# Kernel optimization log

Measured on AMD Instinct MI355X. Metric: run time of the kernel, lower is better.

The kernel has to match this reference:

```python
import jax, jax.numpy as jnp
import numpy as np

N_NODES = 10000
N_EDGES = 160000
D = 512
DROPOUT_P = 0.5
NEG_SLOPE = 0.25


def setup_inputs() -> dict:
    key = jax.random.key(0)
    ks = jax.random.split(key, 8)
    H = jax.random.normal(ks[0], (N_NODES, D), dtype=jnp.float32)
    rows = jax.random.randint(ks[1], (N_EDGES,), 0, N_NODES)
    cols = jax.random.randint(ks[2], (N_EDGES,), 0, N_NODES)
    vals = jax.random.uniform(ks[3], (N_EDGES,), dtype=jnp.float32)
    # xavier-normal-ish weights, zero bias (matches torch init)
    std = float(np.sqrt(2.0 / (D + D)))
    W1 = jax.random.normal(ks[4], (D, D), dtype=jnp.float32) * std
    b1 = jnp.zeros((D,), dtype=jnp.float32)
    W2 = jax.random.normal(ks[5], (D, D), dtype=jnp.float32) * std
    b2 = jnp.zeros((D,), dtype=jnp.float32)
    return {"H": H, "rows": rows, "cols": cols, "vals": vals,
            "W1": W1, "b1": b1, "W2": W2, "b2": b2}


def _spmm(rows, cols, vals, dense):
    # sparse [N,N] @ dense [N,D] via gather + segment-sum
    gathered = vals[:, None] * dense[cols]          # [E, D]
    return jax.ops.segment_sum(gathered, rows, num_segments=N_NODES)


def _leaky_relu(x):
    return jnp.where(x >= 0, x, NEG_SLOPE * x)


def reference(H, rows, cols, vals, W1, b1, W2, b2):
    # layer 1: dense GEMM -> SpMM -> bias -> leaky_relu -> dropout(training=True)
    h = _spmm(rows, cols, vals, H @ W1) + b1
    h = _leaky_relu(h)
    keep = jax.random.bernoulli(jax.random.key(42), 1.0 - DROPOUT_P, h.shape)
    h = jnp.where(keep, h / (1.0 - DROPOUT_P), 0.0)
    # layer 2
    h = _spmm(rows, cols, vals, h @ W2) + b2
    return _leaky_relu(h)
```

## Files before the change

### kernel.cpp

```cpp
#include <hip/hip_runtime.h>
#include <stdint.h>

#define N_NODES 10000
#define M_PAD   10112
#define N_EDGES 160000
#define DIM     512
#define N_ELEMS 5120000
#define NEG_SLOPE 0.25f

typedef short     short8 __attribute__((ext_vector_type(8)));
typedef __bf16    bf16x8 __attribute__((ext_vector_type(8)));
typedef float     f32x4  __attribute__((ext_vector_type(4)));

__device__ __forceinline__ unsigned short f2bf(float f) {
    uint32_t u = __builtin_bit_cast(uint32_t, f);
    uint32_t r = (u + 0x7fffu + ((u >> 16) & 1u)) >> 16;
    return (unsigned short)r;
}
__device__ __forceinline__ float b2f(unsigned short u) {
    return __builtin_bit_cast(float, (uint32_t)u << 16);
}

__device__ __forceinline__ uint32_t rotl32(uint32_t x, uint32_t d) {
    return (x << d) | (x >> (32u - d));
}
__device__ __forceinline__ void threefry_42(uint32_t x0, uint32_t x1,
                                            uint32_t& o0, uint32_t& o1) {
    const uint32_t ks0 = 0u, ks1 = 42u, ks2 = 0x1BD11BDAu ^ 42u;
    x0 += ks0; x1 += ks1;
#define TF_R4(a,b,c,d) \
    x0 += x1; x1 = rotl32(x1,a); x1 ^= x0; \
    x0 += x1; x1 = rotl32(x1,b); x1 ^= x0; \
    x0 += x1; x1 = rotl32(x1,c); x1 ^= x0; \
    x0 += x1; x1 = rotl32(x1,d); x1 ^= x0;
    TF_R4(13,15,26,6);  x0 += ks1; x1 += ks2 + 1u;
    TF_R4(17,29,16,24); x0 += ks2; x1 += ks0 + 2u;
    TF_R4(13,15,26,6);  x0 += ks0; x1 += ks1 + 3u;
    TF_R4(17,29,16,24); x0 += ks1; x1 += ks2 + 4u;
    TF_R4(13,15,26,6);  x0 += ks2; x1 += ks0 + 5u;
#undef TF_R4
    o0 = x0; o1 = x1;
}

__global__ void hist_kernel(const int* __restrict__ rows, int* __restrict__ cnt) {
    int e = blockIdx.x * blockDim.x + threadIdx.x;
    if (e < N_EDGES) atomicAdd(&cnt[rows[e]], 1);
}

__global__ __launch_bounds__(1024)
void scan_kernel(const int* __restrict__ cnt, int* __restrict__ rs, int* __restrict__ cur) {
    __shared__ int s[1024];
    int t = threadIdx.x;
    int base_i = t * 10;
    int local[10];
    int p = 0;
    if (t < 1000) {
        #pragma unroll
        for (int j = 0; j < 10; ++j) { local[j] = cnt[base_i + j]; p += local[j]; }
    }
    s[t] = p;
    __syncthreads();
    for (int off = 1; off < 1024; off <<= 1) {
        int v = (t >= off) ? s[t - off] : 0;
        __syncthreads();
        s[t] += v;
        __syncthreads();
    }
    if (t < 1000) {
        int run = s[t] - p;
        #pragma unroll
        for (int j = 0; j < 10; ++j) {
            rs[base_i + j]  = run;
            cur[base_i + j] = run;
            run += local[j];
        }
        if (t == 999) rs[N_NODES] = run;
    }
}

__global__ void scatter_kernel(const int* __restrict__ rows, const int* __restrict__ cols,
                               const float* __restrict__ vals, int* __restrict__ cur,
                               int* __restrict__ scol, float* __restrict__ sval) {
    int e = blockIdx.x * blockDim.x + threadIdx.x;
    if (e < N_EDGES) {
        int r = rows[e];
        int p = atomicAdd(&cur[r], 1);
        scol[p] = cols[e];
        sval[p] = vals[e];
    }
}

__global__ void convert_kernel(const float* __restrict__ src, unsigned short* __restrict__ dst) {
    int i = blockIdx.x * blockDim.x + threadIdx.x;
    if (i * 4 >= N_ELEMS) return;
    float4 v = ((const float4*)src)[i];
    ushort4 o;
    o.x = f2bf(v.x); o.y = f2bf(v.y); o.z = f2bf(v.z); o.w = f2bf(v.w);
    ((ushort4*)dst)[i] = o;
}

__global__ __launch_bounds__(256)
void transpose_kernel(const float* __restrict__ W, unsigned short* __restrict__ WT) {
    __shared__ float t[64][65];
    int k0 = blockIdx.x * 64, n0 = blockIdx.y * 64;
    int tx = threadIdx.x & 15, ty = threadIdx.x >> 4;
    #pragma unroll
    for (int i = 0; i < 4; ++i) {
        int k = i * 16 + ty;
        float4 v = *(const float4*)&W[(size_t)(k0 + k) * DIM + n0 + tx * 4];
        t[k][tx * 4 + 0] = v.x; t[k][tx * 4 + 1] = v.y;
        t[k][tx * 4 + 2] = v.z; t[k][tx * 4 + 3] = v.w;
    }
    __syncthreads();
    #pragma unroll
    for (int i = 0; i < 4; ++i) {
        int n = i * 16 + ty;
        ushort4 o;
        o.x = f2bf(t[tx * 4 + 0][n]); o.y = f2bf(t[tx * 4 + 1][n]);
        o.z = f2bf(t[tx * 4 + 2][n]); o.w = f2bf(t[tx * 4 + 3][n]);
        *(ushort4*)&WT[(size_t)(n0 + n) * DIM + k0 + tx * 4] = o;
    }
}

__global__ __launch_bounds__(256)
void mfma_gemm(const unsigned short* __restrict__ A, const unsigned short* __restrict__ BT,
               unsigned short* __restrict__ C, int M) {
    __shared__ short8 As[1024];
    __shared__ short8 Bs[1024];
    int tid  = threadIdx.x;
    int wid  = tid >> 6, lane = tid & 63;
    int bm   = blockIdx.x * 128;
    int bn   = blockIdx.y * 128;
    int wm   = (wid >> 1) * 64, wn = (wid & 1) * 64;

    f32x4 acc[4][4] = {};

    int srow = lane >> 3;
    int sslot = lane & 7;

    for (int k0 = 0; k0 < DIM; k0 += 64) {
        #pragma unroll
        for (int c = 0; c < 4; ++c) {
            int chunk = wid * 4 + c;
            int r  = chunk * 8 + srow;
            int ks = sslot ^ (r & 7);
            const unsigned short* ga = A  + (size_t)(bm + r) * DIM + k0 + ks * 8;
            const unsigned short* gb = BT + (size_t)(bn + r) * DIM + k0 + ks * 8;
            __builtin_amdgcn_global_load_lds(
                (const __attribute__((address_space(1))) void*)ga,
                (__attribute__((address_space(3))) void*)&As[chunk * 64], 16, 0, 0);
            __builtin_amdgcn_global_load_lds(
                (const __attribute__((address_space(1))) void*)gb,
                (__attribute__((address_space(3))) void*)&Bs[chunk * 64], 16, 0, 0);
        }
        __syncthreads();

        int lrow = lane & 15;
        int kgrp = lane >> 4;
        #pragma unroll
        for (int ks = 0; ks < 2; ++ks) {
            short8 af[4], bfr[4];
            #pragma unroll
            for (int i = 0; i < 4; ++i) {
                int r = wm + i * 16 + lrow;
                af[i]  = As[r * 8 + ((ks * 4 + kgrp) ^ (r & 7))];
                int n = wn + i * 16 + lrow;
                bfr[i] = Bs[n * 8 + ((ks * 4 + kgrp) ^ (n & 7))];
            }
            #pragma unroll
            for (int i = 0; i < 4; ++i)
                #pragma unroll
                for (int j = 0; j < 4; ++j)
                    acc[i][j] = __builtin_amdgcn_mfma_f32_16x16x32_bf16(
                        __builtin_bit_cast(bf16x8, af[i]),
                        __builtin_bit_cast(bf16x8, bfr[j]), acc[i][j], 0, 0, 0);
        }
        __syncthreads();
    }

    int crow = (lane >> 4) * 4;
    int ccol = lane & 15;
    #pragma unroll
    for (int i = 0; i < 4; ++i) {
        #pragma unroll
        for (int r = 0; r < 4; ++r) {
            int row = bm + wm + i * 16 + crow + r;
            if (row < M) {
                size_t base = (size_t)row * DIM + bn + wn + ccol;
                #pragma unroll
                for (int j = 0; j < 4; ++j)
                    C[base + j * 16] = f2bf(acc[i][j][r]);
            }
        }
    }
}

__global__ __launch_bounds__(128)
void spmm1_kernel(const unsigned short* __restrict__ X, const int* __restrict__ rs,
                  const int* __restrict__ scol, const float* __restrict__ sval,
                  const float* __restrict__ bias, unsigned short* __restrict__ hout) {
    int row = blockIdx.x;
    int t = threadIdx.x;
    int start = rs[row], end = rs[row + 1];
    const ushort4* X4 = (const ushort4*)X;
    float a0 = 0.f, a1 = 0.f, a2 = 0.f, a3 = 0.f;
    float c0 = 0.f, c1 = 0.f, c2 = 0.f, c3 = 0.f;
    int p = start;
    for (; p + 1 < end; p += 2) {
        int   i0 = scol[p], i1 = scol[p + 1];
        float v0 = sval[p], v1 = sval[p + 1];
        ushort4 x0 = X4[(size_t)i0 * 128 + t];
        ushort4 x1 = X4[(size_t)i1 * 128 + t];
        a0 = fmaf(v0, b2f(x0.x), a0); a1 = fmaf(v0, b2f(x0.y), a1);
        a2 = fmaf(v0, b2f(x0.z), a2); a3 = fmaf(v0, b2f(x0.w), a3);
        c0 = fmaf(v1, b2f(x1.x), c0); c1 = fmaf(v1, b2f(x1.y), c1);
        c2 = fmaf(v1, b2f(x1.z), c2); c3 = fmaf(v1, b2f(x1.w), c3);
    }
    if (p < end) {
        int i0 = scol[p]; float v0 = sval[p];
        ushort4 x0 = X4[(size_t)i0 * 128 + t];
        a0 = fmaf(v0, b2f(x0.x), a0); a1 = fmaf(v0, b2f(x0.y), a1);
        a2 = fmaf(v0, b2f(x0.z), a2); a3 = fmaf(v0, b2f(x0.w), a3);
    }
    float r[4];
    float4 b = *(const float4*)&bias[t * 4];
    r[0] = a0 + c0 + b.x; r[1] = a1 + c1 + b.y;
    r[2] = a2 + c2 + b.z; r[3] = a3 + c3 + b.w;
    uint32_t e0 = (uint32_t)row * DIM + t * 4;
    #pragma unroll
    for (int j = 0; j < 4; ++j) {
        float v = r[j];
        v = (v >= 0.f) ? v : NEG_SLOPE * v;
        uint32_t o0, o1;
        threefry_42(0u, e0 + j, o0, o1);
        uint32_t bits = o0 ^ o1;
        r[j] = ((int)bits >= 0) ? v * 2.0f : 0.0f;
    }
    ushort4 o;
    o.x = f2bf(r[0]); o.y = f2bf(r[1]); o.z = f2bf(r[2]); o.w = f2bf(r[3]);
    ((ushort4*)hout)[(size_t)row * 128 + t] = o;
}

__global__ __launch_bounds__(128)
void spmm2_kernel(const unsigned short* __restrict__ X, const int* __restrict__ rs,
                  const int* __restrict__ scol, const float* __restrict__ sval,
                  const float* __restrict__ bias, float* __restrict__ out) {
    int row = blockIdx.x;
    int t = threadIdx.x;
    int start = rs[row], end = rs[row + 1];
    const ushort4* X4 = (const ushort4*)X;
    float a0 = 0.f, a1 = 0.f, a2 = 0.f, a3 = 0.f;
    float c0 = 0.f, c1 = 0.f, c2 = 0.f, c3 = 0.f;
    int p = start;
    for (; p + 1 < end; p += 2) {
        int   i0 = scol[p], i1 = scol[p + 1];
        float v0 = sval[p], v1 = sval[p + 1];
        ushort4 x0 = X4[(size_t)i0 * 128 + t];
        ushort4 x1 = X4[(size_t)i1 * 128 + t];
        a0 = fmaf(v0, b2f(x0.x), a0); a1 = fmaf(v0, b2f(x0.y), a1);
        a2 = fmaf(v0, b2f(x0.z), a2); a3 = fmaf(v0, b2f(x0.w), a3);
        c0 = fmaf(v1, b2f(x1.x), c0); c1 = fmaf(v1, b2f(x1.y), c1);
        c2 = fmaf(v1, b2f(x1.z), c2); c3 = fmaf(v1, b2f(x1.w), c3);
    }
    if (p < end) {
        int i0 = scol[p]; float v0 = sval[p];
        ushort4 x0 = X4[(size_t)i0 * 128 + t];
        a0 = fmaf(v0, b2f(x0.x), a0); a1 = fmaf(v0, b2f(x0.y), a1);
        a2 = fmaf(v0, b2f(x0.z), a2); a3 = fmaf(v0, b2f(x0.w), a3);
    }
    float4 b = *(const float4*)&bias[t * 4];
    float4 r;
    r.x = a0 + c0 + b.x; r.y = a1 + c1 + b.y;
    r.z = a2 + c2 + b.z; r.w = a3 + c3 + b.w;
    r.x = (r.x >= 0.f) ? r.x : NEG_SLOPE * r.x;
    r.y = (r.y >= 0.f) ? r.y : NEG_SLOPE * r.y;
    r.z = (r.z >= 0.f) ? r.z : NEG_SLOPE * r.z;
    r.w = (r.w >= 0.f) ? r.w : NEG_SLOPE * r.w;
    ((float4*)out)[(size_t)row * 128 + t] = r;
}

extern "C" void kernel_launch(void* const* d_in, const int* in_sizes, int n_in,
                              void* d_out, int out_size, void* d_ws, size_t ws_size,
                              hipStream_t stream) {
    const float* H    = (const float*)d_in[0];
    const int*   rows = (const int*)  d_in[1];
    const int*   cols = (const int*)  d_in[2];
    const float* vals = (const float*)d_in[3];
    const float* W1   = (const float*)d_in[4];
    const float* b1   = (const float*)d_in[5];
    const float* W2   = (const float*)d_in[6];
    const float* b2   = (const float*)d_in[7];
    float* out = (float*)d_out;

    char* ws = (char*)d_ws;
    size_t off = 0;
    auto alloc = [&](size_t bytes) -> void* {
        off = (off + 255) & ~(size_t)255;
        void* p = ws + off;
        off += bytes;
        return p;
    };
    int*   cnt  = (int*)  alloc((size_t)N_NODES * 4);
    int*   rs   = (int*)  alloc((size_t)(N_NODES + 1) * 4);
    int*   cur  = (int*)  alloc((size_t)N_NODES * 4);
    int*   scol = (int*)  alloc((size_t)N_EDGES * 4);
    float* sval = (float*)alloc((size_t)N_EDGES * 4);
    unsigned short* WT1 = (unsigned short*)alloc((size_t)DIM * DIM * 2);
    unsigned short* WT2 = (unsigned short*)alloc((size_t)DIM * DIM * 2);
    unsigned short* Abf = (unsigned short*)alloc((size_t)M_PAD * DIM * 2);
    unsigned short* hbf = (unsigned short*)alloc((size_t)M_PAD * DIM * 2);
    unsigned short* Xbf = (unsigned short*)alloc((size_t)N_NODES * DIM * 2);

    convert_kernel<<<(N_ELEMS / 4 + 255) / 256, 256, 0, stream>>>(H, Abf);
    dim3 tgrid(DIM / 64, DIM / 64);
    transpose_kernel<<<tgrid, 256, 0, stream>>>(W1, WT1);
    transpose_kernel<<<tgrid, 256, 0, stream>>>(W2, WT2);
    hipMemsetAsync(cnt, 0, (size_t)N_NODES * 4, stream);
    hist_kernel<<<(N_EDGES + 255) / 256, 256, 0, stream>>>(rows, cnt);
    scan_kernel<<<1, 1024, 0, stream>>>(cnt, rs, cur);
    scatter_kernel<<<(N_EDGES + 255) / 256, 256, 0, stream>>>(rows, cols, vals, cur, scol, sval);

    dim3 ggrid(M_PAD / 128, DIM / 128);
    mfma_gemm<<<ggrid, 256, 0, stream>>>(Abf, WT1, Xbf, N_NODES);
    spmm1_kernel<<<N_NODES, 128, 0, stream>>>(Xbf, rs, scol, sval, b1, hbf);
    mfma_gemm<<<ggrid, 256, 0, stream>>>(hbf, WT2, Xbf, N_NODES);
    spmm2_kernel<<<N_NODES, 128, 0, stream>>>(Xbf, rs, scol, sval, b2, out);
}
```

Before: 126.9 us.

## Fuse prep kernels, precompute dropout mask, shrink GEMM tile, wave-per-row SpMM

```diff
diff --git a/kernel.cpp b/kernel.cpp
--- a/kernel.cpp
+++ b/kernel.cpp
@@ -8,9 +8,10 @@
 #define N_ELEMS 5120000
 #define NEG_SLOPE 0.25f
 
-typedef short     short8 __attribute__((ext_vector_type(8)));
-typedef __bf16    bf16x8 __attribute__((ext_vector_type(8)));
-typedef float     f32x4  __attribute__((ext_vector_type(4)));
+typedef short          short8   __attribute__((ext_vector_type(8)));
+typedef unsigned short ushort8v __attribute__((ext_vector_type(8)));
+typedef __bf16         bf16x8   __attribute__((ext_vector_type(8)));
+typedef float          f32x4    __attribute__((ext_vector_type(4)));
 
 __device__ __forceinline__ unsigned short f2bf(float f) {
     uint32_t u = __builtin_bit_cast(uint32_t, f);
@@ -42,6 +43,71 @@
     o0 = x0; o1 = x1;
 }
 
+#define CONV_BLKS 5000
+#define TR_BLKS   64
+#define MASK_BLKS 625
+#define ZERO_BLKS 10
+
+__device__ __forceinline__ void transpose_tile(const float* __restrict__ W,
+                                               unsigned short* __restrict__ WT,
+                                               int tile, float (*ts)[65]) {
+    int k0 = (tile & 7) * 64, n0 = (tile >> 3) * 64;
+    int tx = threadIdx.x & 15, ty = threadIdx.x >> 4;
+    #pragma unroll
+    for (int i = 0; i < 4; ++i) {
+        int k = i * 16 + ty;
+        float4 v = *(const float4*)&W[(size_t)(k0 + k) * DIM + n0 + tx * 4];
+        ts[k][tx * 4 + 0] = v.x; ts[k][tx * 4 + 1] = v.y;
+        ts[k][tx * 4 + 2] = v.z; ts[k][tx * 4 + 3] = v.w;
+    }
+    __syncthreads();
+    #pragma unroll
+    for (int i = 0; i < 4; ++i) {
+        int n = i * 16 + ty;
+        ushort4 o;
+        o.x = f2bf(ts[tx * 4 + 0][n]); o.y = f2bf(ts[tx * 4 + 1][n]);
+        o.z = f2bf(ts[tx * 4 + 2][n]); o.w = f2bf(ts[tx * 4 + 3][n]);
+        *(ushort4*)&WT[(size_t)(n0 + n) * DIM + k0 + tx * 4] = o;
+    }
+}
+
+__global__ __launch_bounds__(256)
+void prep_kernel(const float* __restrict__ H, const float* __restrict__ W1,
+                 const float* __restrict__ W2, unsigned short* __restrict__ Abf,
+                 unsigned short* __restrict__ WT1, unsigned short* __restrict__ WT2,
+                 uint32_t* __restrict__ mask, int* __restrict__ cnt) {
+    __shared__ float ts[64][65];
+    int b = blockIdx.x;
+    if (b < CONV_BLKS) {
+        int i = b * 256 + threadIdx.x;
+        float4 v = ((const float4*)H)[i];
+        ushort4 o;
+        o.x = f2bf(v.x); o.y = f2bf(v.y); o.z = f2bf(v.z); o.w = f2bf(v.w);
+        ((ushort4*)Abf)[i] = o;
+    } else if (b < CONV_BLKS + TR_BLKS) {
+        transpose_tile(W1, WT1, b - CONV_BLKS, ts);
+    } else if (b < CONV_BLKS + 2 * TR_BLKS) {
+        transpose_tile(W2, WT2, b - CONV_BLKS - TR_BLKS, ts);
+    } else if (b < CONV_BLKS + 2 * TR_BLKS + MASK_BLKS) {
+        int w = (b - CONV_BLKS - 2 * TR_BLKS) * 256 + threadIdx.x;
+        uint32_t base = (uint32_t)w * 32;
+        uint32_t m = 0;
+        #pragma unroll
+        for (int j = 0; j < 32; ++j) {
+            uint32_t o0, o1;
+            threefry_42(0u, base + j, o0, o1);
+            uint32_t bits = o0 ^ o1;
+            m |= (uint32_t)(((int)bits >= 0) ? 1u : 0u) << j;
+        }
+        mask[w] = m;
+    } else {
+        int i = (b - CONV_BLKS - 2 * TR_BLKS - MASK_BLKS) * 1024 + threadIdx.x * 4;
+        #pragma unroll
+        for (int j = 0; j < 4; ++j)
+            if (i + j < N_NODES) cnt[i + j] = 0;
+    }
+}
+
 __global__ void hist_kernel(const int* __restrict__ rows, int* __restrict__ cnt) {
     int e = blockIdx.x * blockDim.x + threadIdx.x;
     if (e < N_EDGES) atomicAdd(&cnt[rows[e]], 1);
@@ -90,68 +156,40 @@
     }
 }
 
-__global__ void convert_kernel(const float* __restrict__ src, unsigned short* __restrict__ dst) {
-    int i = blockIdx.x * blockDim.x + threadIdx.x;
-    if (i * 4 >= N_ELEMS) return;
-    float4 v = ((const float4*)src)[i];
-    ushort4 o;
-    o.x = f2bf(v.x); o.y = f2bf(v.y); o.z = f2bf(v.z); o.w = f2bf(v.w);
-    ((ushort4*)dst)[i] = o;
-}
-
-__global__ __launch_bounds__(256)
-void transpose_kernel(const float* __restrict__ W, unsigned short* __restrict__ WT) {
-    __shared__ float t[64][65];
-    int k0 = blockIdx.x * 64, n0 = blockIdx.y * 64;
-    int tx = threadIdx.x & 15, ty = threadIdx.x >> 4;
-    #pragma unroll
-    for (int i = 0; i < 4; ++i) {
-        int k = i * 16 + ty;
-        float4 v = *(const float4*)&W[(size_t)(k0 + k) * DIM + n0 + tx * 4];
-        t[k][tx * 4 + 0] = v.x; t[k][tx * 4 + 1] = v.y;
-        t[k][tx * 4 + 2] = v.z; t[k][tx * 4 + 3] = v.w;
-    }
-    __syncthreads();
-    #pragma unroll
-    for (int i = 0; i < 4; ++i) {
-        int n = i * 16 + ty;
-        ushort4 o;
-        o.x = f2bf(t[tx * 4 + 0][n]); o.y = f2bf(t[tx * 4 + 1][n]);
-        o.z = f2bf(t[tx * 4 + 2][n]); o.w = f2bf(t[tx * 4 + 3][n]);
-        *(ushort4*)&WT[(size_t)(n0 + n) * DIM + k0 + tx * 4] = o;
-    }
-}
-
 __global__ __launch_bounds__(256)
 void mfma_gemm(const unsigned short* __restrict__ A, const unsigned short* __restrict__ BT,
                unsigned short* __restrict__ C, int M) {
-    __shared__ short8 As[1024];
-    __shared__ short8 Bs[1024];
+    __shared__ short8 As[128 * 8];
+    __shared__ short8 Bs[64 * 8];
     int tid  = threadIdx.x;
     int wid  = tid >> 6, lane = tid & 63;
     int bm   = blockIdx.x * 128;
-    int bn   = blockIdx.y * 128;
-    int wm   = (wid >> 1) * 64, wn = (wid & 1) * 64;
-
-    f32x4 acc[4][4] = {};
-
-    int srow = lane >> 3;
-    int sslot = lane & 7;
+    int bn   = blockIdx.y * 64;
+    int wm   = (wid >> 1) * 64, wn = (wid & 1) * 32;
+
+    f32x4 acc[4][2] = {};
+    int srow = lane >> 3, sslot = lane & 7;
 
     for (int k0 = 0; k0 < DIM; k0 += 64) {
         #pragma unroll
         for (int c = 0; c < 4; ++c) {
-            int chunk = wid * 4 + c;
-            int r  = chunk * 8 + srow;
+            int r0 = c * 32 + wid * 8;
+            int r  = r0 + srow;
             int ks = sslot ^ (r & 7);
-            const unsigned short* ga = A  + (size_t)(bm + r) * DIM + k0 + ks * 8;
+            const unsigned short* ga = A + (size_t)(bm + r) * DIM + k0 + ks * 8;
+            __builtin_amdgcn_global_load_lds(
+                (const __attribute__((address_space(1))) void*)ga,
+                (__attribute__((address_space(3))) void*)&As[r0 * 8], 16, 0, 0);
+        }
+        #pragma unroll
+        for (int c = 0; c < 2; ++c) {
+            int r0 = c * 32 + wid * 8;
+            int r  = r0 + srow;
+            int ks = sslot ^ (r & 7);
             const unsigned short* gb = BT + (size_t)(bn + r) * DIM + k0 + ks * 8;
             __builtin_amdgcn_global_load_lds(
-                (const __attribute__((address_space(1))) void*)ga,
-                (__attribute__((address_space(3))) void*)&As[chunk * 64], 16, 0, 0);
-            __builtin_amdgcn_global_load_lds(
                 (const __attribute__((address_space(1))) void*)gb,
-                (__attribute__((address_space(3))) void*)&Bs[chunk * 64], 16, 0, 0);
+                (__attribute__((address_space(3))) void*)&Bs[r0 * 8], 16, 0, 0);
         }
         __syncthreads();
 
@@ -159,18 +197,21 @@
         int kgrp = lane >> 4;
         #pragma unroll
         for (int ks = 0; ks < 2; ++ks) {
-            short8 af[4], bfr[4];
+            short8 af[4], bfr[2];
             #pragma unroll
             for (int i = 0; i < 4; ++i) {
                 int r = wm + i * 16 + lrow;
-                af[i]  = As[r * 8 + ((ks * 4 + kgrp) ^ (r & 7))];
-                int n = wn + i * 16 + lrow;
-                bfr[i] = Bs[n * 8 + ((ks * 4 + kgrp) ^ (n & 7))];
+                af[i] = As[r * 8 + ((ks * 4 + kgrp) ^ (r & 7))];
+            }
+            #pragma unroll
+            for (int j = 0; j < 2; ++j) {
+                int n = wn + j * 16 + lrow;
+                bfr[j] = Bs[n * 8 + ((ks * 4 + kgrp) ^ (n & 7))];
             }
             #pragma unroll
             for (int i = 0; i < 4; ++i)
                 #pragma unroll
-                for (int j = 0; j < 4; ++j)
+                for (int j = 0; j < 2; ++j)
                     acc[i][j] = __builtin_amdgcn_mfma_f32_16x16x32_bf16(
                         __builtin_bit_cast(bf16x8, af[i]),
                         __builtin_bit_cast(bf16x8, bfr[j]), acc[i][j], 0, 0, 0);
@@ -188,95 +229,103 @@
             if (row < M) {
                 size_t base = (size_t)row * DIM + bn + wn + ccol;
                 #pragma unroll
-                for (int j = 0; j < 4; ++j)
+                for (int j = 0; j < 2; ++j)
                     C[base + j * 16] = f2bf(acc[i][j][r]);
             }
         }
     }
 }
 
-__global__ __launch_bounds__(128)
+__global__ __launch_bounds__(256)
 void spmm1_kernel(const unsigned short* __restrict__ X, const int* __restrict__ rs,
                   const int* __restrict__ scol, const float* __restrict__ sval,
-                  const float* __restrict__ bias, unsigned short* __restrict__ hout) {
-    int row = blockIdx.x;
-    int t = threadIdx.x;
+                  const float* __restrict__ bias, const uint8_t* __restrict__ mask,
+                  unsigned short* __restrict__ hout) {
+    int row  = blockIdx.x * 4 + (threadIdx.x >> 6);
+    int lane = threadIdx.x & 63;
     int start = rs[row], end = rs[row + 1];
-    const ushort4* X4 = (const ushort4*)X;
-    float a0 = 0.f, a1 = 0.f, a2 = 0.f, a3 = 0.f;
-    float c0 = 0.f, c1 = 0.f, c2 = 0.f, c3 = 0.f;
+    const ushort8v* X8 = (const ushort8v*)X;
+    float a[8] = {}, b[8] = {};
     int p = start;
-    for (; p + 1 < end; p += 2) {
-        int   i0 = scol[p], i1 = scol[p + 1];
-        float v0 = sval[p], v1 = sval[p + 1];
-        ushort4 x0 = X4[(size_t)i0 * 128 + t];
-        ushort4 x1 = X4[(size_t)i1 * 128 + t];
-        a0 = fmaf(v0, b2f(x0.x), a0); a1 = fmaf(v0, b2f(x0.y), a1);
-        a2 = fmaf(v0, b2f(x0.z), a2); a3 = fmaf(v0, b2f(x0.w), a3);
-        c0 = fmaf(v1, b2f(x1.x), c0); c1 = fmaf(v1, b2f(x1.y), c1);
-        c2 = fmaf(v1, b2f(x1.z), c2); c3 = fmaf(v1, b2f(x1.w), c3);
-    }
-    if (p < end) {
-        int i0 = scol[p]; float v0 = sval[p];
-        ushort4 x0 = X4[(size_t)i0 * 128 + t];
-        a0 = fmaf(v0, b2f(x0.x), a0); a1 = fmaf(v0, b2f(x0.y), a1);
-        a2 = fmaf(v0, b2f(x0.z), a2); a3 = fmaf(v0, b2f(x0.w), a3);
-    }
-    float r[4];
-    float4 b = *(const float4*)&bias[t * 4];
-    r[0] = a0 + c0 + b.x; r[1] = a1 + c1 + b.y;
-    r[2] = a2 + c2 + b.z; r[3] = a3 + c3 + b.w;
-    uint32_t e0 = (uint32_t)row * DIM + t * 4;
-    #pragma unroll
-    for (int j = 0; j < 4; ++j) {
-        float v = r[j];
+    for (; p + 3 < end; p += 4) {
+        int   c0 = scol[p],     c1 = scol[p + 1], c2 = scol[p + 2], c3 = scol[p + 3];
+        float v0 = sval[p],     v1 = sval[p + 1], v2 = sval[p + 2], v3 = sval[p + 3];
+        ushort8v x0 = X8[(size_t)c0 * 64 + lane];
+        ushort8v x1 = X8[(size_t)c1 * 64 + lane];
+        ushort8v x2 = X8[(size_t)c2 * 64 + lane];
+        ushort8v x3 = X8[(size_t)c3 * 64 + lane];
+        #pragma unroll
+        for (int e = 0; e < 8; ++e) {
+            a[e] = fmaf(v0, b2f(x0[e]), a[e]);
+            b[e] = fmaf(v1, b2f(x1[e]), b[e]);
+            a[e] = fmaf(v2, b2f(x2[e]), a[e]);
+            b[e] = fmaf(v3, b2f(x3[e]), b[e]);
+        }
+    }
+    for (; p < end; ++p) {
+        int c0 = scol[p]; float v0 = sval[p];
+        ushort8v x0 = X8[(size_t)c0 * 64 + lane];
+        #pragma unroll
+        for (int e = 0; e < 8; ++e) a[e] = fmaf(v0, b2f(x0[e]), a[e]);
+    }
+    float4 bi0 = ((const float4*)bias)[lane * 2];
+    float4 bi1 = ((const float4*)bias)[lane * 2 + 1];
+    float bb[8] = { bi0.x, bi0.y, bi0.z, bi0.w, bi1.x, bi1.y, bi1.z, bi1.w };
+    uint32_t mb = mask[(size_t)row * 64 + lane];
+    ushort8v o;
+    #pragma unroll
+    for (int e = 0; e < 8; ++e) {
+        float v = a[e] + b[e] + bb[e];
         v = (v >= 0.f) ? v : NEG_SLOPE * v;
-        uint32_t o0, o1;
-        threefry_42(0u, e0 + j, o0, o1);
-        uint32_t bits = o0 ^ o1;
-        r[j] = ((int)bits >= 0) ? v * 2.0f : 0.0f;
-    }
-    ushort4 o;
-    o.x = f2bf(r[0]); o.y = f2bf(r[1]); o.z = f2bf(r[2]); o.w = f2bf(r[3]);
-    ((ushort4*)hout)[(size_t)row * 128 + t] = o;
-}
-
-__global__ __launch_bounds__(128)
+        v = ((mb >> e) & 1u) ? v * 2.0f : 0.0f;
+        o[e] = f2bf(v);
+    }
+    ((ushort8v*)hout)[(size_t)row * 64 + lane] = o;
+}
+
+__global__ __launch_bounds__(256)
 void spmm2_kernel(const unsigned short* __restrict__ X, const int* __restrict__ rs,
                   const int* __restrict__ scol, const float* __restrict__ sval,
                   const float* __restrict__ bias, float* __restrict__ out) {
-    int row = blockIdx.x;
-    int t = threadIdx.x;
+    int row  = blockIdx.x * 4 + (threadIdx.x >> 6);
+    int lane = threadIdx.x & 63;
     int start = rs[row], end = rs[row + 1];
-    const ushort4* X4 = (const ushort4*)X;
-    float a0 = 0.f, a1 = 0.f, a2 = 0.f, a3 = 0.f;
-    float c0 = 0.f, c1 = 0.f, c2 = 0.f, c3 = 0.f;
+    const ushort8v* X8 = (const ushort8v*)X;
+    float a[8] = {}, b[8] = {};
     int p = start;
-    for (; p + 1 < end; p += 2) {
-        int   i0 = scol[p], i1 = scol[p + 1];
-        float v0 = sval[p], v1 = sval[p + 1];
-        ushort4 x0 = X4[(size_t)i0 * 128 + t];
-        ushort4 x1 = X4[(size_t)i1 * 128 + t];
-        a0 = fmaf(v0, b2f(x0.x), a0); a1 = fmaf(v0, b2f(x0.y), a1);
-        a2 = fmaf(v0, b2f(x0.z), a2); a3 = fmaf(v0, b2f(x0.w), a3);
-        c0 = fmaf(v1, b2f(x1.x), c0); c1 = fmaf(v1, b2f(x1.y), c1);
-        c2 = fmaf(v1, b2f(x1.z), c2); c3 = fmaf(v1, b2f(x1.w), c3);
-    }
-    if (p < end) {
-        int i0 = scol[p]; float v0 = sval[p];
-        ushort4 x0 = X4[(size_t)i0 * 128 + t];
-        a0 = fmaf(v0, b2f(x0.x), a0); a1 = fmaf(v0, b2f(x0.y), a1);
-        a2 = fmaf(v0, b2f(x0.z), a2); a3 = fmaf(v0, b2f(x0.w), a3);
-    }
-    float4 b = *(const float4*)&bias[t * 4];
-    float4 r;
-    r.x = a0 + c0 + b.x; r.y = a1 + c1 + b.y;
-    r.z = a2 + c2 + b.z; r.w = a3 + c3 + b.w;
-    r.x = (r.x >= 0.f) ? r.x : NEG_SLOPE * r.x;
-    r.y = (r.y >= 0.f) ? r.y : NEG_SLOPE * r.y;
-    r.z = (r.z >= 0.f) ? r.z : NEG_SLOPE * r.z;
-    r.w = (r.w >= 0.f) ? r.w : NEG_SLOPE * r.w;
-    ((float4*)out)[(size_t)row * 128 + t] = r;
+    for (; p + 3 < end; p += 4) {
+        int   c0 = scol[p],     c1 = scol[p + 1], c2 = scol[p + 2], c3 = scol[p + 3];
+        float v0 = sval[p],     v1 = sval[p + 1], v2 = sval[p + 2], v3 = sval[p + 3];
+        ushort8v x0 = X8[(size_t)c0 * 64 + lane];
+        ushort8v x1 = X8[(size_t)c1 * 64 + lane];
+        ushort8v x2 = X8[(size_t)c2 * 64 + lane];
+        ushort8v x3 = X8[(size_t)c3 * 64 + lane];
+        #pragma unroll
+        for (int e = 0; e < 8; ++e) {
+            a[e] = fmaf(v0, b2f(x0[e]), a[e]);
+            b[e] = fmaf(v1, b2f(x1[e]), b[e]);
+            a[e] = fmaf(v2, b2f(x2[e]), a[e]);
+            b[e] = fmaf(v3, b2f(x3[e]), b[e]);
+        }
+    }
+    for (; p < end; ++p) {
+        int c0 = scol[p]; float v0 = sval[p];
+        ushort8v x0 = X8[(size_t)c0 * 64 + lane];
+        #pragma unroll
+        for (int e = 0; e < 8; ++e) a[e] = fmaf(v0, b2f(x0[e]), a[e]);
+    }
+    float4 bi0 = ((const float4*)bias)[lane * 2];
+    float4 bi1 = ((const float4*)bias)[lane * 2 + 1];
+    float r[8] = { bi0.x, bi0.y, bi0.z, bi0.w, bi1.x, bi1.y, bi1.z, bi1.w };
+    #pragma unroll
+    for (int e = 0; e < 8; ++e) {
+        float v = a[e] + b[e] + r[e];
+        r[e] = (v >= 0.f) ? v : NEG_SLOPE * v;
+    }
+    float4 o0 = make_float4(r[0], r[1], r[2], r[3]);
+    float4 o1 = make_float4(r[4], r[5], r[6], r[7]);
+    ((float4*)out)[(size_t)row * 128 + lane * 2]     = o0;
+    ((float4*)out)[(size_t)row * 128 + lane * 2 + 1] = o1;
 }
 
 extern "C" void kernel_launch(void* const* d_in, const int* in_sizes, int n_in,
@@ -300,29 +349,28 @@
         off += bytes;
         return p;
     };
-    int*   cnt  = (int*)  alloc((size_t)N_NODES * 4);
-    int*   rs   = (int*)  alloc((size_t)(N_NODES + 1) * 4);
-    int*   cur  = (int*)  alloc((size_t)N_NODES * 4);
-    int*   scol = (int*)  alloc((size_t)N_EDGES * 4);
-    float* sval = (float*)alloc((size_t)N_EDGES * 4);
+    int*      cnt  = (int*)     alloc((size_t)N_NODES * 4);
+    int*      rs   = (int*)     alloc((size_t)(N_NODES + 1) * 4);
+    int*      cur  = (int*)     alloc((size_t)N_NODES * 4);
+    int*      scol = (int*)     alloc((size_t)N_EDGES * 4);
+    float*    sval = (float*)   alloc((size_t)N_EDGES * 4);
+    uint32_t* mask = (uint32_t*)alloc((size_t)N_ELEMS / 8);
     unsigned short* WT1 = (unsigned short*)alloc((size_t)DIM * DIM * 2);
     unsigned short* WT2 = (unsigned short*)alloc((size_t)DIM * DIM * 2);
     unsigned short* Abf = (unsigned short*)alloc((size_t)M_PAD * DIM * 2);
     unsigned short* hbf = (unsigned short*)alloc((size_t)M_PAD * DIM * 2);
     unsigned short* Xbf = (unsigned short*)alloc((size_t)N_NODES * DIM * 2);
 
-    convert_kernel<<<(N_ELEMS / 4 + 255) / 256, 256, 0, stream>>>(H, Abf);
-    dim3 tgrid(DIM / 64, DIM / 64);
-    transpose_kernel<<<tgrid, 256, 0, stream>>>(W1, WT1);
-    transpose_kernel<<<tgrid, 256, 0, stream>>>(W2, WT2);
-    hipMemsetAsync(cnt, 0, (size_t)N_NODES * 4, stream);
+    int prep_blocks = CONV_BLKS + 2 * TR_BLKS + MASK_BLKS + ZERO_BLKS;
+    prep_kernel<<<prep_blocks, 256, 0, stream>>>(H, W1, W2, Abf, WT1, WT2, mask, cnt);
     hist_kernel<<<(N_EDGES + 255) / 256, 256, 0, stream>>>(rows, cnt);
     scan_kernel<<<1, 1024, 0, stream>>>(cnt, rs, cur);
     scatter_kernel<<<(N_EDGES + 255) / 256, 256, 0, stream>>>(rows, cols, vals, cur, scol, sval);
 
-    dim3 ggrid(M_PAD / 128, DIM / 128);
+    dim3 ggrid(M_PAD / 128, DIM / 64);
     mfma_gemm<<<ggrid, 256, 0, stream>>>(Abf, WT1, Xbf, N_NODES);
-    spmm1_kernel<<<N_NODES, 128, 0, stream>>>(Xbf, rs, scol, sval, b1, hbf);
+    spmm1_kernel<<<N_NODES / 4, 256, 0, stream>>>(Xbf, rs, scol, sval, b1,
+                                                  (const uint8_t*)mask, hbf);
     mfma_gemm<<<ggrid, 256, 0, stream>>>(hbf, WT2, Xbf, N_NODES);
-    spmm2_kernel<<<N_NODES, 128, 0, stream>>>(Xbf, rs, scol, sval, b2, out);
-}
+    spmm2_kernel<<<N_NODES / 4, 256, 0, stream>>>(Xbf, rs, scol, sval, b2, out);
+}
```

After: 137.3 us. +8.2%, slower.
